# Optimization experiments

Hardware: AMD Instinct MI355X
Metric: run time of the kernel (lower is better)

## Reference

```python
import jax, jax.numpy as jnp
import numpy as np

N_NODES = 50000
N_EDGES = 800000
IN_CH = 256
HID_CH = 128


def setup_inputs() -> dict:
    key = jax.random.key(0)
    k1, k2, k3, k4, k5 = jax.random.split(key, 5)
    x = jax.random.normal(k1, (N_NODES, IN_CH), dtype=jnp.float32)
    edge_index = jax.random.randint(k2, (2, N_EDGES), 0, N_NODES, dtype=jnp.int64)
    edge_weight = jax.random.uniform(k3, (N_EDGES,), dtype=jnp.float32)
    W = jax.random.normal(k4, (IN_CH, HID_CH), dtype=jnp.float32) * (1.0 / np.sqrt(IN_CH))
    b = jnp.zeros((HID_CH,), dtype=jnp.float32)
    alpha = jnp.full((HID_CH,), 0.25, dtype=jnp.float32)  # PReLU default init
    return {"x": x, "edge_index": edge_index, "edge_weight": edge_weight,
            "W": W, "b": b, "alpha": alpha}


def reference(x, edge_index, edge_weight, W, b, alpha):
    """GCNConv (with self-loops + symmetric normalization) followed by PReLU."""
    N = x.shape[0]
    row, col = edge_index[0], edge_index[1]
    # add self-loops with weight 1 (PyG gcn_norm default, add_self_loops=True)
    loop = jnp.arange(N, dtype=row.dtype)
    row = jnp.concatenate([row, loop])
    col = jnp.concatenate([col, loop])
    ew = jnp.concatenate([edge_weight, jnp.ones((N,), dtype=edge_weight.dtype)])
    # degree from edge weights, scattered at destination (col)
    deg = jax.ops.segment_sum(ew, col, num_segments=N)
    deg_inv_sqrt = jnp.where(deg > 0, jax.lax.rsqrt(deg), 0.0)
    norm = deg_inv_sqrt[row] * ew * deg_inv_sqrt[col]  # [E+N]
    # linear transform then gather-scale-scatter aggregation
    h = x @ W                               # [N, HID]
    msg = h[row] * norm[:, None]            # [E+N, HID]
    out = jax.ops.segment_sum(msg, col, num_segments=N) + b
    # PReLU with per-channel slope
    return jnp.where(out >= 0, out, alpha * out)
```

## Files before the change

kernel.cpp:

```cpp
#include <hip/hip_runtime.h>

#define NN 50000
#define NE 800000
#define KD 256
#define CD 128
#define NB 196
#define GEMM_BLOCKS 782
#define HIST_BLOCKS 3125

typedef __attribute__((ext_vector_type(8))) short short8;
typedef __attribute__((ext_vector_type(4))) float floatx4;

__device__ inline unsigned short f2bf(float f) {
    unsigned u = __float_as_uint(f);
    unsigned r = (u + 0x7FFFu + ((u >> 16) & 1u)) >> 16;
    return (unsigned short)r;
}
__device__ inline float bf2f_lo(unsigned u) { return __uint_as_float(u << 16); }
__device__ inline float bf2f_hi(unsigned u) { return __uint_as_float(u & 0xFFFF0000u); }

__global__ __launch_bounds__(256) void prep(const float* __restrict__ W,
                                            unsigned short* __restrict__ Wt,
                                            unsigned* __restrict__ packedAll,
                                            unsigned long long* __restrict__ state) {
    __shared__ unsigned short t[32][33];
    if (blockIdx.x < NB) {
        const int g = blockIdx.x * 256 + threadIdx.x;
        if (g < NN) {
#pragma unroll
            for (int c = 0; c < 4; c++) packedAll[(size_t)c * NN + g] = 0u;
        }
        if (blockIdx.x == 0) {
            for (int i = threadIdx.x; i < NB * 8; i += 256) state[i] = 0ull;
        }
        return;
    }
    const int b2 = blockIdx.x - NB;
    const int bk = (b2 & 7) * 32;
    const int bn = (b2 >> 3) * 32;
    const int tx = threadIdx.x & 31;
    const int ty = threadIdx.x >> 5;
#pragma unroll
    for (int i = 0; i < 32; i += 8)
        t[ty + i][tx] = f2bf(W[(size_t)(bk + ty + i) * CD + bn + tx]);
    __syncthreads();
#pragma unroll
    for (int i = 0; i < 32; i += 8)
        Wt[(size_t)(bn + ty + i) * KD + bk + tx] = t[tx][ty + i];
}

__global__ __launch_bounds__(256) void fused_gemm_hist(
        const float* __restrict__ x, const unsigned short* __restrict__ Wt,
        unsigned short* __restrict__ hb,
        const int* __restrict__ col, const float* __restrict__ ew,
        unsigned* __restrict__ packedAll, unsigned short* __restrict__ rank) {
    __shared__ unsigned short As[64][40];
    __shared__ unsigned short Bs[128][40];

    if (blockIdx.x >= GEMM_BLOCKS) {
        const int hblk = blockIdx.x - GEMM_BLOCKS;
        const int e = hblk * 256 + threadIdx.x;
        if (e < NE) {
            unsigned* packed = packedAll + (size_t)(hblk & 3) * NN;
            unsigned p = (1u << 24) + (unsigned)(ew[e] * 262144.0f);
            unsigned old = atomicAdd(&packed[col[e]], p);
            rank[e] = (unsigned short)(old >> 24);
        }
        return;
    }

    const int tid  = threadIdx.x;
    const int wave = tid >> 6;
    const int lane = tid & 63;
    const int row0 = blockIdx.x * 64;
    const int m0   = wave * 16;
    const int lr   = lane & 15;
    const int quad = lane >> 4;

    const int ar = tid >> 2;
    const int aq = tid & 3;
    const int bn = tid >> 1;
    const int bh = (tid & 1) * 16;

    const int gr = row0 + ar;
    const bool ok = gr < NN;
    const float* xb = x + (size_t)gr * KD + aq * 8;
    const unsigned short* wb = Wt + (size_t)bn * KD + bh;

    floatx4 acc[8];
#pragma unroll
    for (int nt = 0; nt < 8; nt++) acc[nt] = (floatx4){0.f, 0.f, 0.f, 0.f};

    float4 f0 = {0.f, 0.f, 0.f, 0.f}, f1 = {0.f, 0.f, 0.f, 0.f};
    short8 wv0, wv1;
    if (ok) { f0 = *(const float4*)xb; f1 = *(const float4*)(xb + 4); }
    wv0 = *(const short8*)wb;
    wv1 = *(const short8*)(wb + 8);

#pragma unroll
    for (int kt = 0; kt < 8; kt++) {
        union { short8 v; unsigned short us[8]; } av;
        if (ok) {
            av.us[0] = f2bf(f0.x); av.us[1] = f2bf(f0.y);
            av.us[2] = f2bf(f0.z); av.us[3] = f2bf(f0.w);
            av.us[4] = f2bf(f1.x); av.us[5] = f2bf(f1.y);
            av.us[6] = f2bf(f1.z); av.us[7] = f2bf(f1.w);
        } else {
            av.v = (short8){0,0,0,0,0,0,0,0};
        }
        *(short8*)&As[ar][aq * 8] = av.v;
        *(short8*)&Bs[bn][bh]     = wv0;
        *(short8*)&Bs[bn][bh + 8] = wv1;
        __syncthreads();
        if (kt < 7) {
            const float* xp = xb + (kt + 1) * 32;
            if (ok) { f0 = *(const float4*)xp; f1 = *(const float4*)(xp + 4); }
            const unsigned short* wp = wb + (kt + 1) * 32;
            wv0 = *(const short8*)wp;
            wv1 = *(const short8*)(wp + 8);
        }
        short8 af = *(const short8*)&As[m0 + lr][quad * 8];
#pragma unroll
        for (int nt = 0; nt < 8; nt++) {
            short8 bfr = *(const short8*)&Bs[nt * 16 + lr][quad * 8];
            acc[nt] = __builtin_amdgcn_mfma_f32_16x16x32_bf16(af, bfr, acc[nt], 0, 0, 0);
        }
        __syncthreads();
    }

#pragma unroll
    for (int i = 0; i < 4; i++) {
        const int grow = row0 + m0 + quad * 4 + i;
        if (grow < NN) {
            unsigned short* hp = hb + (size_t)grow * CD + lr;
#pragma unroll
            for (int nt = 0; nt < 8; nt++)
                hp[nt * 16] = f2bf(acc[nt][i]);
        }
    }
}

__global__ __launch_bounds__(256) void scan_lookback(
        const unsigned* __restrict__ packedAll,
        unsigned long long* __restrict__ state,
        int* __restrict__ start, int4* __restrict__ base4,
        float* __restrict__ dinv) {
    __shared__ int sm[256];
    __shared__ int sbase;
    const int t = threadIdx.x;
    const int b = blockIdx.x;
    const int g = b * 256 + t;

    int cc[4] = {0, 0, 0, 0};
    unsigned lowsum = 0;
    int v = 0;
    if (g < NN) {
#pragma unroll
        for (int c = 0; c < 4; c++) {
            unsigned p = packedAll[(size_t)c * NN + g];
            cc[c] = (int)(p >> 24);
            lowsum += p & 0xFFFFFFu;
            v += cc[c];
        }
    }
    sm[t] = v;
    __syncthreads();
#pragma unroll
    for (int off = 1; off < 256; off <<= 1) {
        int u = (t >= off) ? sm[t - off] : 0;
        __syncthreads();
        sm[t] += u;
        __syncthreads();
    }
    const int incl = sm[t];
    const int total = sm[255];

    if (t == 0) {
        if (b == 0) {
            __hip_atomic_store(&state[0], (2ull << 32) | (unsigned)total,
                               __ATOMIC_RELAXED, __HIP_MEMORY_SCOPE_AGENT);
            sbase = 0;
        } else {
            __hip_atomic_store(&state[(size_t)b * 8], (1ull << 32) | (unsigned)total,
                               __ATOMIC_RELAXED, __HIP_MEMORY_SCOPE_AGENT);
            long long run = 0;
            int i = b - 1;
            while (true) {
                unsigned long long s = __hip_atomic_load(&state[(size_t)i * 8],
                                        __ATOMIC_RELAXED, __HIP_MEMORY_SCOPE_AGENT);
                unsigned st = (unsigned)(s >> 32);
                if (st == 0u) { __builtin_amdgcn_s_sleep(1); continue; }
                run += (unsigned)s;
                if (st == 2u) break;
                i--;
            }
            __hip_atomic_store(&state[(size_t)b * 8],
                               (2ull << 32) | (unsigned)(run + total),
                               __ATOMIC_RELAXED, __HIP_MEMORY_SCOPE_AGENT);
            sbase = (int)run;
        }
    }
    __syncthreads();
    const int base = sbase;

    if (g < NN) {
        const int s = base + (incl - v);
        start[g] = s;
        base4[g] = make_int4(s, s + cc[0], s + cc[0] + cc[1], s + cc[0] + cc[1] + cc[2]);
        float degs = (float)lowsum * (1.0f / 262144.0f);
        dinv[g] = rsqrtf(1.0f + degs);
    }
    if (g == 0) start[NN] = NE;
}

__global__ __launch_bounds__(256) void meta_write(const int* __restrict__ row,
                                                  const int* __restrict__ col,
                                                  const float* __restrict__ ew,
                                                  const unsigned short* __restrict__ rank,
                                                  const int4* __restrict__ base4,
                                                  const float* __restrict__ dinv,
                                                  unsigned* __restrict__ meta) {
    const int e = blockIdx.x * 256 + threadIdx.x;
    if (e >= NE) return;
    const int copy = blockIdx.x & 3;
    const int c = col[e];
    const int r = row[e];
    int4 b4 = base4[c];
    int base = (copy == 0) ? b4.x : (copy == 1) ? b4.y : (copy == 2) ? b4.z : b4.w;
    int pos = base + rank[e];
    unsigned short wbf = f2bf(dinv[r] * ew[e]);
    meta[pos] = ((unsigned)wbf << 16) | (unsigned)r;
}

__global__ __launch_bounds__(256) void aggregate(const int* __restrict__ start,
                                                 const unsigned* __restrict__ meta,
                                                 const unsigned short* __restrict__ hb,
                                                 const float* __restrict__ dinv,
                                                 const float* __restrict__ bias,
                                                 const float* __restrict__ alpha,
                                                 float* __restrict__ out) {
    int n = blockIdx.x * 4 + (threadIdx.x >> 6);
    if (n >= NN) return;
    n = __builtin_amdgcn_readfirstlane(n);
    const int lane = threadIdx.x & 63;
    const int s = __builtin_amdgcn_readfirstlane(start[n]);
    const int e = __builtin_amdgcn_readfirstlane(start[n + 1]);

    float A0[8], A1[8];
#pragma unroll
    for (int j = 0; j < 8; j++) { A0[j] = 0.f; A1[j] = 0.f; }

    int i = s;
    for (; i + 8 <= e; i += 8) {
        unsigned m[8], u[8];
#pragma unroll
        for (int j = 0; j < 8; j++) m[j] = meta[i + j];
#pragma unroll
        for (int j = 0; j < 8; j++)
            u[j] = *(const unsigned*)(hb + (size_t)(m[j] & 0xFFFFu) * CD + lane * 2);
#pragma unroll
        for (int j = 0; j < 8; j++) {
            float w = __uint_as_float(m[j] & 0xFFFF0000u);
            A0[j] = fmaf(w, bf2f_lo(u[j]), A0[j]);
            A1[j] = fmaf(w, bf2f_hi(u[j]), A1[j]);
        }
    }
    for (; i < e; i++) {
        unsigned m = meta[i];
        unsigned u = *(const unsigned*)(hb + (size_t)(m & 0xFFFFu) * CD + lane * 2);
        float w = __uint_as_float(m & 0xFFFF0000u);
        A0[0] = fmaf(w, bf2f_lo(u), A0[0]);
        A1[0] = fmaf(w, bf2f_hi(u), A1[0]);
    }
#pragma unroll
    for (int j = 1; j < 8; j++) { A0[0] += A0[j]; A1[0] += A1[j]; }

    const float dc = dinv[n];
    unsigned us = *(const unsigned*)(hb + (size_t)n * CD + lane * 2);
    const int ch = lane * 2;
    float o0 = dc * A0[0] + dc * dc * bf2f_lo(us) + bias[ch];
    float o1 = dc * A1[0] + dc * dc * bf2f_hi(us) + bias[ch + 1];
    o0 = o0 >= 0.f ? o0 : alpha[ch] * o0;
    o1 = o1 >= 0.f ? o1 : alpha[ch + 1] * o1;
    *(float2*)(out + (size_t)n * CD + ch) = make_float2(o0, o1);
}

extern "C" void kernel_launch(void* const* d_in, const int* in_sizes, int n_in,
                              void* d_out, int out_size, void* d_ws, size_t ws_size,
                              hipStream_t stream) {
    const float* x     = (const float*)d_in[0];
    const int*   eidx  = (const int*)d_in[1];
    const float* ew    = (const float*)d_in[2];
    const float* Wm    = (const float*)d_in[3];
    const float* bias  = (const float*)d_in[4];
    const float* alpha = (const float*)d_in[5];
    const int* row = eidx;
    const int* col = eidx + NE;

    float* out = (float*)d_out;

    char* ws = (char*)d_ws;
    unsigned* packedAll = (unsigned*)(ws);
    int*   start    = (int*)(ws + 800000);
    float* dinv     = (float*)(ws + 1000064);
    unsigned short* rank = (unsigned short*)(ws + 1200064);
    int4*  base4    = (int4*)(ws + 2800064);
    unsigned* meta  = (unsigned*)(ws + 3600064);
    unsigned short* Wt = (unsigned short*)(ws + 6800064);
    unsigned long long* state = (unsigned long long*)(ws + 6865600);
    unsigned short* hb = (unsigned short*)(ws + 6878208);

    prep          <<<NB + 32, 256, 0, stream>>>(Wm, Wt, packedAll, state);
    fused_gemm_hist<<<GEMM_BLOCKS + HIST_BLOCKS, 256, 0, stream>>>(
                        x, Wt, hb, col, ew, packedAll, rank);
    scan_lookback <<<NB, 256, 0, stream>>>(packedAll, state, start, base4, dinv);
    meta_write    <<<HIST_BLOCKS, 256, 0, stream>>>(row, col, ew, rank, base4, dinv, meta);
    aggregate     <<<(NN + 3) / 4, 256, 0, stream>>>(start, meta, hb, dinv, bias, alpha, out);
}
```

Baseline: 193.6 us.

## Parallelize scan lookback across a wavefront, vectorize meta_write, use nontemporal accesses

The decoupled lookback in the scan now has a whole 64-lane wavefront read 64 predecessor states at once, using ballots and shuffle reductions instead of a single thread walking back one block at a time. meta_write handles four edges per thread with vector loads of col, row, weight and rank, and launches a quarter as many blocks. The copy index is derived from e>>8 so it matches the original per-block assignment. aggregate reads meta and writes the output with nontemporal hints to reduce cache pollution. These are several unrelated tweaks, and the lookback logic is more complex and harder to verify.

After: 186.2 us. 1.04x faster.

```diff
diff --git a/kernel.cpp b/kernel.cpp
--- a/kernel.cpp
+++ b/kernel.cpp
@@ -7,9 +7,11 @@
 #define NB 196
 #define GEMM_BLOCKS 782
 #define HIST_BLOCKS 3125
+#define META_BLOCKS 782
 
 typedef __attribute__((ext_vector_type(8))) short short8;
 typedef __attribute__((ext_vector_type(4))) float floatx4;
+typedef __attribute__((ext_vector_type(2))) float floatx2;
 
 __device__ inline unsigned short f2bf(float f) {
     unsigned u = __float_as_uint(f);
@@ -176,24 +178,51 @@
     const int total = sm[255];
 
     if (t == 0) {
-        if (b == 0) {
-            __hip_atomic_store(&state[0], (2ull << 32) | (unsigned)total,
-                               __ATOMIC_RELAXED, __HIP_MEMORY_SCOPE_AGENT);
-            sbase = 0;
-        } else {
-            __hip_atomic_store(&state[(size_t)b * 8], (1ull << 32) | (unsigned)total,
-                               __ATOMIC_RELAXED, __HIP_MEMORY_SCOPE_AGENT);
-            long long run = 0;
-            int i = b - 1;
-            while (true) {
-                unsigned long long s = __hip_atomic_load(&state[(size_t)i * 8],
-                                        __ATOMIC_RELAXED, __HIP_MEMORY_SCOPE_AGENT);
-                unsigned st = (unsigned)(s >> 32);
-                if (st == 0u) { __builtin_amdgcn_s_sleep(1); continue; }
-                run += (unsigned)s;
-                if (st == 2u) break;
-                i--;
+        unsigned long long post =
+            ((b == 0 ? 2ull : 1ull) << 32) | (unsigned)total;
+        __hip_atomic_store(&state[(size_t)b * 8], post,
+                           __ATOMIC_RELAXED, __HIP_MEMORY_SCOPE_AGENT);
+        if (b == 0) sbase = 0;
+    }
+    if (b > 0 && t < 64) {
+        long long run = 0;
+        int i = b - 1;
+        while (true) {
+            const int idx = i - t;
+            unsigned long long s = (idx >= 0)
+                ? __hip_atomic_load(&state[(size_t)idx * 8],
+                                    __ATOMIC_RELAXED, __HIP_MEMORY_SCOPE_AGENT)
+                : (2ull << 32);
+            const unsigned st = (unsigned)(s >> 32);
+            const unsigned long long b0m = __ballot(st == 0u);
+            const unsigned long long b2m = __ballot(st == 2u);
+            if (b2m) {
+                const int L = __ffsll((long long)b2m) - 1;
+                const unsigned long long below =
+                    (L == 63) ? ~0ull : ((1ull << (L + 1)) - 1ull);
+                if (b0m & below) { __builtin_amdgcn_s_sleep(1); continue; }
+                unsigned val = (t <= L) ? (unsigned)s : 0u;
+#pragma unroll
+                for (int o = 32; o; o >>= 1) val += __shfl_xor(val, o);
+                run += val;
+                break;
+            } else if (b0m) {
+                const int L0 = __ffsll((long long)b0m) - 1;
+                unsigned val = (t < L0) ? (unsigned)s : 0u;
+#pragma unroll
+                for (int o = 32; o; o >>= 1) val += __shfl_xor(val, o);
+                run += val;
+                i -= L0;
+                if (L0 == 0) __builtin_amdgcn_s_sleep(1);
+            } else {
+                unsigned val = (unsigned)s;
+#pragma unroll
+                for (int o = 32; o; o >>= 1) val += __shfl_xor(val, o);
+                run += val;
+                i -= 64;
             }
+        }
+        if (t == 0) {
             __hip_atomic_store(&state[(size_t)b * 8],
                                (2ull << 32) | (unsigned)(run + total),
                                __ATOMIC_RELAXED, __HIP_MEMORY_SCOPE_AGENT);
@@ -220,16 +249,26 @@
                                                   const int4* __restrict__ base4,
                                                   const float* __restrict__ dinv,
                                                   unsigned* __restrict__ meta) {
-    const int e = blockIdx.x * 256 + threadIdx.x;
-    if (e >= NE) return;
-    const int copy = blockIdx.x & 3;
-    const int c = col[e];
-    const int r = row[e];
-    int4 b4 = base4[c];
-    int base = (copy == 0) ? b4.x : (copy == 1) ? b4.y : (copy == 2) ? b4.z : b4.w;
-    int pos = base + rank[e];
-    unsigned short wbf = f2bf(dinv[r] * ew[e]);
-    meta[pos] = ((unsigned)wbf << 16) | (unsigned)r;
+    const int e0 = (blockIdx.x * 256 + threadIdx.x) * 4;
+    if (e0 >= NE) return;
+    const int4 c4 = *(const int4*)(col + e0);
+    const int4 r4 = *(const int4*)(row + e0);
+    const float4 w4 = *(const float4*)(ew + e0);
+    const ushort4 k4 = *(const ushort4*)(rank + e0);
+    const int cs[4] = {c4.x, c4.y, c4.z, c4.w};
+    const int rs[4] = {r4.x, r4.y, r4.z, r4.w};
+    const float wsv[4] = {w4.x, w4.y, w4.z, w4.w};
+    const unsigned short ks[4] = {k4.x, k4.y, k4.z, k4.w};
+#pragma unroll
+    for (int j = 0; j < 4; j++) {
+        const int e = e0 + j;
+        const int copy = (e >> 8) & 3;
+        const int4 b4 = base4[cs[j]];
+        const int base = (copy == 0) ? b4.x : (copy == 1) ? b4.y
+                       : (copy == 2) ? b4.z : b4.w;
+        const unsigned short wbf = f2bf(dinv[rs[j]] * wsv[j]);
+        meta[base + ks[j]] = ((unsigned)wbf << 16) | (unsigned)rs[j];
+    }
 }
 
 __global__ __launch_bounds__(256) void aggregate(const int* __restrict__ start,
@@ -254,7 +293,7 @@
     for (; i + 8 <= e; i += 8) {
         unsigned m[8], u[8];
 #pragma unroll
-        for (int j = 0; j < 8; j++) m[j] = meta[i + j];
+        for (int j = 0; j < 8; j++) m[j] = __builtin_nontemporal_load(meta + i + j);
 #pragma unroll
         for (int j = 0; j < 8; j++)
             u[j] = *(const unsigned*)(hb + (size_t)(m[j] & 0xFFFFu) * CD + lane * 2);
@@ -266,7 +305,7 @@
         }
     }
     for (; i < e; i++) {
-        unsigned m = meta[i];
+        unsigned m = __builtin_nontemporal_load(meta + i);
         unsigned u = *(const unsigned*)(hb + (size_t)(m & 0xFFFFu) * CD + lane * 2);
         float w = __uint_as_float(m & 0xFFFF0000u);
         A0[0] = fmaf(w, bf2f_lo(u), A0[0]);
@@ -282,7 +321,8 @@
     float o1 = dc * A1[0] + dc * dc * bf2f_hi(us) + bias[ch + 1];
     o0 = o0 >= 0.f ? o0 : alpha[ch] * o0;
     o1 = o1 >= 0.f ? o1 : alpha[ch + 1] * o1;
-    *(float2*)(out + (size_t)n * CD + ch) = make_float2(o0, o1);
+    floatx2 o; o.x = o0; o.y = o1;
+    __builtin_nontemporal_store(o, (floatx2*)(out + (size_t)n * CD + ch));
 }
 
 extern "C" void kernel_launch(void* const* d_in, const int* in_sizes, int n_in,
@@ -314,6 +354,6 @@
     fused_gemm_hist<<<GEMM_BLOCKS + HIST_BLOCKS, 256, 0, stream>>>(
                         x, Wt, hb, col, ew, packedAll, rank);
     scan_lookback <<<NB, 256, 0, stream>>>(packedAll, state, start, base4, dinv);
-    meta_write    <<<HIST_BLOCKS, 256, 0, stream>>>(row, col, ew, rank, base4, dinv, meta);
+    meta_write    <<<META_BLOCKS, 256, 0, stream>>>(row, col, ew, rank, base4, dinv, meta);
     aggregate     <<<(NN + 3) / 4, 256, 0, stream>>>(start, meta, hb, dinv, bias, alpha, out);
 }
```
